# Kernel optimization log

Hardware: AMD Instinct MI355X
Metric: run time of the kernel (lower is better)

Reference implementation:

```python
import jax, jax.numpy as jnp
import numpy as np

B, N, G, H = 64, 1000, 500, 256
TANH_CLIP = 10.0


def setup_inputs() -> dict:
    key = jax.random.key(0)
    ks = jax.random.split(key, 8)
    embeddings = jax.random.normal(ks[0], (B, N, H), dtype=jnp.float32)
    dists = jax.random.uniform(ks[1], (B, N, N), dtype=jnp.float32)
    last_node = jax.random.randint(ks[2], (B, G), 0, N)
    visited = jax.random.uniform(ks[3], (B, G, N)) < 0.3
    group_ninf_mask = jnp.where(visited, -jnp.inf, 0.0).astype(jnp.float32)
    s = 1.0 / np.sqrt(H)
    Wq_graph = jax.random.normal(ks[4], (H, H), dtype=jnp.float32) * s
    Wq_first = jax.random.normal(ks[5], (H, H), dtype=jnp.float32) * s
    Wq_last = jax.random.normal(ks[6], (H, H), dtype=jnp.float32) * s
    W_visited = jax.random.normal(ks[7], (H, H), dtype=jnp.float32) * s
    return dict(embeddings=embeddings, dists=dists, last_node=last_node,
                group_ninf_mask=group_ninf_mask, Wq_graph=Wq_graph,
                Wq_first=Wq_first, Wq_last=Wq_last, W_visited=W_visited)


def reference(embeddings, dists, last_node, group_ninf_mask,
              Wq_graph, Wq_first, Wq_last, W_visited) -> jnp.ndarray:
    b, n, h = embeddings.shape
    g = last_node.shape[1]
    inv_sqrt_h = 1.0 / np.float32(np.sqrt(h))
    inv_sqrt_2 = np.float32(1.0 / np.sqrt(2.0))

    # reset(): graph query from mean-pooled embeddings  [B,1,H]
    q_graph = jnp.einsum('bih,oh->bio', embeddings.mean(axis=1, keepdims=True), Wq_graph)

    # gather last-node embeddings  [B,G,H]
    idx = jnp.broadcast_to(last_node[:, :, None], (b, g, h))
    last_emb = jnp.take_along_axis(embeddings, idx, axis=1)
    q_last = jnp.einsum('bgh,oh->bgo', last_emb, Wq_last)
    # first call: q_first built from the same last-node embedding
    q_first = jnp.einsum('bgh,oh->bgo', last_emb, Wq_first)

    # visited-set query: mask (-inf->1) @ embeddings / N, then linear
    mask_visited = jnp.where(jnp.isneginf(group_ninf_mask), 1.0, group_ninf_mask)
    pooled = jnp.einsum('bgn,bnh->bgh', mask_visited, embeddings) / np.float32(n)
    q_visited = jnp.einsum('bgh,oh->bgo', pooled, W_visited)

    # distances from last node to all nodes  [B,G,N]
    didx = jnp.broadcast_to(last_node[:, :, None], (b, g, n))
    distances = jnp.take_along_axis(dists, didx, axis=1)

    final_q = q_last + q_first + q_graph + q_visited  # [B,G,H]
    score = jnp.einsum('bgh,bnh->bgn', final_q, embeddings) * inv_sqrt_h - distances * inv_sqrt_2
    score_clipped = TANH_CLIP * jnp.tanh(score)
    mask_prob = jnp.where(jnp.isneginf(group_ninf_mask), -1e8, group_ninf_mask)
    return jax.nn.softmax(score_clipped + mask_prob, axis=-1)
```

## Files before the change

kernel.cpp:

```cpp
#include <hip/hip_runtime.h>
#include <hip/hip_fp16.h>
#include <math.h>

#define Bb 64
#define Nn 1000
#define Gg 500
#define Hh 256
#define GP 512
#define NP 1024

#define WS_MP   0u
#define WS_RS   262144u
#define WS_BM   294912u
#define WS_WC16 1343488u
#define WS_E16  1409024u
#define WS_T16  9601024u
#define WS_P16  17989632u
#define WS_F16  WS_T16
#define WS_PO   22183936u

typedef __attribute__((ext_vector_type(8))) short short8;
typedef __attribute__((ext_vector_type(8))) _Float16 f16x8;
typedef __attribute__((ext_vector_type(4))) float f32x4;
typedef __attribute__((ext_vector_type(4))) unsigned short u16x4;

#define MFMAH(a,b,c) __builtin_amdgcn_mfma_f32_16x16x32_f16(a,b,c,0,0,0)
#define SW(row, chunk) (((row) << 6) + ((((chunk) ^ ((row) & 7))) << 3))

__device__ __forceinline__ unsigned short f16b(float v) {
  return __half_as_ushort(__float2half(v));
}
__device__ __forceinline__ float h2f(unsigned short u) {
  return __half2float(__ushort_as_half(u));
}

__global__ __launch_bounds__(256) void k_front(const float* __restrict__ emb,
                                               const float* __restrict__ gm,
                                               const float* __restrict__ Wf,
                                               const float* __restrict__ Wl,
                                               const float* __restrict__ Wv,
                                               float* __restrict__ ws) {
  __shared__ float tile[64][68];
  __shared__ float colsum[16][64];
  int bid = blockIdx.x, t = threadIdx.x;
  if (bid < 4096) {
    int nt = bid & 15, ht = (bid >> 4) & 3, b = bid >> 6;
    int c4 = (t & 15) * 4, r0 = t >> 4;
    int n0 = nt * 64, h0 = ht * 64;
    unsigned short* e16 = (unsigned short*)(ws + WS_E16);
    unsigned short* t16 = (unsigned short*)(ws + WS_T16);
    float cs0 = 0.f, cs1 = 0.f, cs2 = 0.f, cs3 = 0.f;
#pragma unroll
    for (int rr = 0; rr < 4; ++rr) {
      int r = r0 + rr * 16;
      int n = n0 + r;
      float4 v = {0.f, 0.f, 0.f, 0.f};
      if (n < Nn) {
        size_t idx = ((size_t)(b * Nn + n)) * Hh + h0 + c4;
        v = *(const float4*)(emb + idx);
        u16x4 e4 = { f16b(v.x), f16b(v.y), f16b(v.z), f16b(v.w) };
        *(u16x4*)(e16 + idx) = e4;
      }
      *(float4*)&tile[r][c4] = v;
      cs0 += v.x; cs1 += v.y; cs2 += v.z; cs3 += v.w;
    }
    colsum[r0][c4 + 0] = cs0; colsum[r0][c4 + 1] = cs1;
    colsum[r0][c4 + 2] = cs2; colsum[r0][c4 + 3] = cs3;
    __syncthreads();
    {
      int h_l = t >> 2, nseg = t & 3;
      short8 h8a, h8b;
#pragma unroll
      for (int i = 0; i < 16; ++i) {
        float v = tile[nseg * 16 + i][h_l];
        unsigned short hv = f16b(v);
        if (i < 8) h8a[i] = (short)hv;
        else       h8b[i-8] = (short)hv;
      }
      size_t base = ((size_t)(b * Hh + h0 + h_l)) * NP + n0 + nseg * 16;
      *(short8*)(t16 + base) = h8a; *(short8*)(t16 + base + 8) = h8b;
    }
    if (t < 64) {
      float s = 0.f;
#pragma unroll
      for (int i = 0; i < 16; ++i) s += colsum[i][t];
      ws[WS_MP + (((size_t)(b * Hh + h0 + t)) << 4) + nt] = s;
    }
  } else if (bid < 12288) {
    int w = t >> 6, l = t & 63;
    int row = (bid - 4096) * 4 + w;
    int b = row >> 9, g = row & 511;
    unsigned long long* dst = (unsigned long long*)((unsigned short*)(ws + WS_BM) + (size_t)row * 64);
    if (g < Gg) {
      const float* src = gm + ((size_t)b * Gg + g) * Nn;
#pragma unroll
      for (int i = 0; i < 16; ++i) {
        int n = i * 64 + l;
        bool bit = (n < Nn) ? (src[n] < -1e30f) : false;
        unsigned long long m = __ballot(bit);
        if (l == i) dst[i] = m;
      }
    } else {
      if (l < 16) dst[l] = 0ull;
    }
  } else if (bid < 12544) {
    int o = bid - 12288, k = t;
    unsigned short* wc = (unsigned short*)(ws + WS_WC16);
    wc[o*512 + k]       = f16b(Wv[o*Hh + k]);
    wc[o*512 + 256 + k] = f16b(Wl[o*Hh + k] + Wf[o*Hh + k]);
  } else {
    ws[WS_RS + (bid - 12544) * 256 + t] = 0.f;
  }
}

__global__ __launch_bounds__(256, 2) void k_pool(float* __restrict__ ws) {
  __shared__ __align__(16) unsigned short sT[128*64];
  int id = blockIdx.x;
  int xcd = id & 7, seq = id >> 3;
  int b = xcd * 8 + (seq >> 3);
  int inner = seq & 7, ht = inner >> 2, gt = inner & 3;
  int t = threadIdx.x, w = t >> 6, lane = t & 63;
  int wh = w >> 1, wg = w & 1, l15 = lane & 15, lk = lane >> 4;
  const unsigned short* t16 = (const unsigned short*)(ws + WS_T16);
  const unsigned short* bmp = (const unsigned short*)(ws + WS_BM);
  unsigned short* p16 = (unsigned short*)(ws + WS_P16);
  int h0 = ht*128, g0 = gt*128;
  f32x4 acc[4][4] = {};
  const unsigned short* brow[4];
#pragma unroll
  for (int fn = 0; fn < 4; ++fn) {
    int g = g0 + wg*64 + fn*16 + l15; if (g > Gg-1) g = Gg-1;
    brow[fn] = bmp + ((size_t)(b*GP + g)) * 64;
  }
  int bitoff = (lk & 1) * 8;
  int srow = t >> 1, sc0 = (t & 1) * 4;
  size_t sbase = ((size_t)(b*Hh + h0 + srow)) * NP;
  for (int st = 0; st < 16; ++st) {
    int k0 = st * 64;
#pragma unroll
    for (int i = 0; i < 4; ++i) {
      int cc = sc0 + i;
      *(short8*)&sT[SW(srow, cc)] = *(const short8*)(t16 + sbase + k0 + cc*8);
    }
    __syncthreads();
#pragma unroll
    for (int kk = 0; kk < 64; kk += 32) {
      f16x8 ah[4], bmf[4];
#pragma unroll
      for (int fm = 0; fm < 4; ++fm)
        ah[fm] = *(const f16x8*)&sT[SW(wh*64 + fm*16 + l15, (kk>>3) + lk)];
#pragma unroll
      for (int fn = 0; fn < 4; ++fn) {
        unsigned c = brow[fn][((k0 + kk) >> 4) + (lk >> 1)];
        short8 bs;
#pragma unroll
        for (int i = 0; i < 8; ++i)
          bs[i] = ((c >> (bitoff + i)) & 1) ? (short)0x3C00 : (short)0;
        bmf[fn] = *(const f16x8*)&bs;
      }
#pragma unroll
      for (int fm = 0; fm < 4; ++fm)
#pragma unroll
        for (int fn = 0; fn < 4; ++fn)
          acc[fm][fn] = MFMAH(ah[fm], bmf[fn], acc[fm][fn]);
    }
    __syncthreads();
  }
#pragma unroll
  for (int fm = 0; fm < 4; ++fm)
#pragma unroll
    for (int fn = 0; fn < 4; ++fn) {
      int h = h0 + wh*64 + fm*16 + lk*4;
      int g = g0 + wg*64 + fn*16 + l15;
      u16x4 v4;
#pragma unroll
      for (int j = 0; j < 4; ++j) v4[j] = f16b(acc[fm][fn][j] * (1.0f/Nn));
      *(u16x4*)(p16 + ((size_t)(b*GP + g)) * Hh + h) = v4;
    }
}

__global__ __launch_bounds__(256, 2) void k_finalq(const int* __restrict__ last_node,
                                                   const float* __restrict__ Wg,
                                                   float* __restrict__ ws) {
  __shared__ __align__(16) unsigned short sA[128*64], sB[128*64];
  __shared__ int lL[128];
  __shared__ float mean[256];
  __shared__ float qv[128];
  int id = blockIdx.x;
  int xcd = id & 7, seq = id >> 3;
  int b = xcd * 8 + (seq >> 3);
  int inner = seq & 7, ot = inner >> 2, gt = inner & 3;
  int t = threadIdx.x, w = t >> 6, lane = t & 63;
  int wo = w >> 1, wg = w & 1, l15 = lane & 15, lk = lane >> 4;
  const unsigned short* wc = (const unsigned short*)(ws + WS_WC16);
  const unsigned short* p16 = (const unsigned short*)(ws + WS_P16);
  const unsigned short* e16 = (const unsigned short*)(ws + WS_E16);
  unsigned short* f16 = (unsigned short*)(ws + WS_F16);
  int o0 = ot*128, g0 = gt*128;
  if (t < 128) lL[t] = last_node[b*Gg + ((g0 + t) < Gg ? (g0 + t) : Gg-1)];
  {
    const float4* mp4 = (const float4*)(ws + WS_MP + (((size_t)(b * Hh + t)) << 4));
    float s = 0.f;
#pragma unroll
    for (int q = 0; q < 4; ++q) {
      float4 v = mp4[q];
      s += v.x + v.y + v.z + v.w;
    }
    mean[t] = s * (1.0f/Nn);
  }
  __syncthreads();
  if (t < 128) {
    const float4* wrow = (const float4*)(Wg + (size_t)(o0 + t) * Hh);
    float a = 0.f;
#pragma unroll
    for (int h4 = 0; h4 < 64; ++h4) {
      float4 wv = wrow[h4];
      a += mean[h4*4]*wv.x + mean[h4*4+1]*wv.y + mean[h4*4+2]*wv.z + mean[h4*4+3]*wv.w;
    }
    qv[t] = a;
  }
  __syncthreads();
  f32x4 acc[4][4] = {};
  int srow = t >> 1, sc0 = (t & 1) * 4;
  size_t abase = ((size_t)(o0 + srow)) * 512;
  size_t pbase = ((size_t)(b*GP + g0 + srow)) * Hh;
  size_t lbase = ((size_t)(b*Nn + lL[srow])) * Hh;
  for (int st = 0; st < 8; ++st) {
    int k0 = st * 64;
#pragma unroll
    for (int i = 0; i < 4; ++i) {
      int cc = sc0 + i;
      int d = SW(srow, cc);
      *(short8*)&sA[d] = *(const short8*)(wc + abase + k0 + cc*8);
      if (k0 < 256)
        *(short8*)&sB[d] = *(const short8*)(p16 + pbase + k0 + cc*8);
      else
        *(short8*)&sB[d] = *(const short8*)(e16 + lbase + (k0 - 256) + cc*8);
    }
    __syncthreads();
#pragma unroll
    for (int kk = 0; kk < 64; kk += 32) {
      f16x8 a[4], bb[4];
#pragma unroll
      for (int fm = 0; fm < 4; ++fm)
        a[fm] = *(const f16x8*)&sA[SW(wo*64 + fm*16 + l15, (kk>>3) + lk)];
#pragma unroll
      for (int fn = 0; fn < 4; ++fn)
        bb[fn] = *(const f16x8*)&sB[SW(wg*64 + fn*16 + l15, (kk>>3) + lk)];
#pragma unroll
      for (int fm = 0; fm < 4; ++fm)
#pragma unroll
        for (int fn = 0; fn < 4; ++fn)
          acc[fm][fn] = MFMAH(a[fm], bb[fn], acc[fm][fn]);
    }
    __syncthreads();
  }
#pragma unroll
  for (int fm = 0; fm < 4; ++fm) {
    int ob = wo*64 + fm*16 + lk*4;
    float q4[4] = { qv[ob+0], qv[ob+1], qv[ob+2], qv[ob+3] };
#pragma unroll
    for (int fn = 0; fn < 4; ++fn) {
      int g = g0 + wg*64 + fn*16 + l15;
      u16x4 v4;
#pragma unroll
      for (int j = 0; j < 4; ++j) v4[j] = f16b(acc[fm][fn][j] + q4[j]);
      *(u16x4*)(f16 + ((size_t)(b*GP + g)) * Hh + o0 + ob) = v4;
    }
  }
}

__global__ __launch_bounds__(256, 4) void k_score(const float* __restrict__ dists,
                                                  const int* __restrict__ last_node,
                                                  float* __restrict__ ws) {
  __shared__ __align__(16) unsigned short sE[128*64], sF[128*64];
  __shared__ int lL[128];
  int id = blockIdx.x;
  int swz = ((id & 7) << 8) | (id >> 3);
  int gt = swz & 3, nt = (swz >> 2) & 7, b = swz >> 5;
  int t = threadIdx.x, w = t >> 6, lane = t & 63;
  int wn = w >> 1, wg = w & 1, l15 = lane & 15, lk = lane >> 4;
  const unsigned short* e16 = (const unsigned short*)(ws + WS_E16);
  const unsigned short* f16 = (const unsigned short*)(ws + WS_F16);
  const unsigned short* bmp = (const unsigned short*)(ws + WS_BM);
  unsigned short* po = (unsigned short*)(ws + WS_PO);
  float* rs = ws + WS_RS;
  int n0 = nt*128, g0 = gt*128;
  if (t < 128) lL[t] = last_node[b*Gg + ((g0 + t) < Gg ? (g0 + t) : Gg-1)];
  __syncthreads();
  f32x4 acc[4][4] = {};
  int srow = t >> 1, sc0 = (t & 1) * 4;
  int nr = n0 + srow; if (nr > Nn-1) nr = Nn-1;
  size_t ebase = ((size_t)(b*Nn + nr)) * Hh;
  size_t fbase = ((size_t)(b*GP + g0 + srow)) * Hh;
  for (int st = 0; st < 4; ++st) {
    int k0 = st * 64;
#pragma unroll
    for (int i = 0; i < 4; ++i) {
      int cc = sc0 + i;
      int d = SW(srow, cc);
      *(short8*)&sE[d] = *(const short8*)(e16 + ebase + k0 + cc*8);
      *(short8*)&sF[d] = *(const short8*)(f16 + fbase + k0 + cc*8);
    }
    __syncthreads();
#pragma unroll
    for (int kk = 0; kk < 64; kk += 32) {
      f16x8 a[4], bb[4];
#pragma unroll
      for (int fm = 0; fm < 4; ++fm)
        a[fm] = *(const f16x8*)&sE[SW(wn*64 + fm*16 + l15, (kk>>3) + lk)];
#pragma unroll
      for (int fn = 0; fn < 4; ++fn)
        bb[fn] = *(const f16x8*)&sF[SW(wg*64 + fn*16 + l15, (kk>>3) + lk)];
#pragma unroll
      for (int fm = 0; fm < 4; ++fm)
#pragma unroll
        for (int fn = 0; fn < 4; ++fn)
          acc[fm][fn] = MFMAH(a[fm], bb[fn], acc[fm][fn]);
    }
    __syncthreads();
  }
  const float c2 = 0.70710678118654752f;
  float rsum[4] = {0.f, 0.f, 0.f, 0.f};
#pragma unroll
  for (int fn = 0; fn < 4; ++fn) {
    int gl = wg*64 + fn*16 + l15;
    int g = g0 + gl;
    if (g < Gg) {
      int L = lL[gl];
      const float* drow = dists + ((size_t)(b*Nn + L)) * Nn;
      const unsigned short* bmr = bmp + ((size_t)(b*GP + g)) * 64;
      unsigned short* prow = po + ((size_t)(b*Gg + g)) * 1024;
#pragma unroll
      for (int fm = 0; fm < 4; ++fm) {
        int n = n0 + wn*64 + fm*16 + lk*4;
        if (n < Nn) {
          float4 d4 = *(const float4*)(drow + n);
          unsigned cb = bmr[n >> 4];
          int bo = n & 15;
          float dd[4] = {d4.x, d4.y, d4.z, d4.w};
          unsigned short h4[4];
#pragma unroll
          for (int j = 0; j < 4; ++j) {
            float s = fmaf(acc[fm][fn][j], 0.0625f, -dd[j] * c2);
            float e = __expf(-2.0f * fabsf(s));
            float r = __builtin_amdgcn_rcpf(1.0f + e);
            float m = fmaf(-20.0f, e * r, 10.0f);
            float parg = copysignf(m, s) - 10.0f;
            float p = ((cb >> (bo + j)) & 1) ? 0.f : __expf(parg);
            rsum[fn] += p;
            h4[j] = f16b(p);
          }
          uint2 u = { (unsigned)h4[0] | ((unsigned)h4[1] << 16),
                      (unsigned)h4[2] | ((unsigned)h4[3] << 16) };
          *(uint2*)(prow + n) = u;
        }
      }
    }
  }
#pragma unroll
  for (int fn = 0; fn < 4; ++fn) {
    rsum[fn] += __shfl_xor(rsum[fn], 16);
    rsum[fn] += __shfl_xor(rsum[fn], 32);
    int g = g0 + wg*64 + fn*16 + l15;
    if (lk == 0 && g < Gg) atomicAdd(rs + b*GP + g, rsum[fn]);
  }
}

__global__ __launch_bounds__(256) void k_norm(const float* __restrict__ ws,
                                              float* __restrict__ out) {
  int id = blockIdx.x, t = threadIdx.x;
  int xcd = id & 7, seq = id >> 3;
  int b = xcd * 8 + (seq >> 8);
  int inner = seq & 255;
  int v = inner * 256 + t;
  if (v >= 62500) return;
  int lg = v / 125;
  int n = (v - lg * 125) * 8;
  const unsigned short* po = (const unsigned short*)(ws + WS_PO);
  size_t bg = (size_t)b * Gg + lg;
  float inv = 1.0f / ws[WS_RS + b*GP + lg];
  uint4 u = *(const uint4*)(po + bg * 1024 + n);
  float* orow = out + bg * Nn + n;
  float4 o0, o1;
  o0.x = h2f((unsigned short)(u.x & 0xFFFF)) * inv;
  o0.y = h2f((unsigned short)(u.x >> 16)) * inv;
  o0.z = h2f((unsigned short)(u.y & 0xFFFF)) * inv;
  o0.w = h2f((unsigned short)(u.y >> 16)) * inv;
  o1.x = h2f((unsigned short)(u.z & 0xFFFF)) * inv;
  o1.y = h2f((unsigned short)(u.z >> 16)) * inv;
  o1.z = h2f((unsigned short)(u.w & 0xFFFF)) * inv;
  o1.w = h2f((unsigned short)(u.w >> 16)) * inv;
  *(float4*)orow = o0;
  *(float4*)(orow + 4) = o1;
}

extern "C" void kernel_launch(void* const* d_in, const int* in_sizes, int n_in,
                              void* d_out, int out_size, void* d_ws, size_t ws_size,
                              hipStream_t stream) {
  const float* emb       = (const float*)d_in[0];
  const float* dists     = (const float*)d_in[1];
  const int*   last_node = (const int*)d_in[2];
  const float* gm        = (const float*)d_in[3];
  const float* Wg        = (const float*)d_in[4];
  const float* Wf        = (const float*)d_in[5];
  const float* Wl        = (const float*)d_in[6];
  const float* Wv        = (const float*)d_in[7];
  float* out = (float*)d_out;
  float* ws  = (float*)d_ws;

  hipLaunchKernelGGL(k_front,  dim3(12672),     dim3(256), 0, stream, emb, gm, Wf, Wl, Wv, ws);
  hipLaunchKernelGGL(k_pool,   dim3(512),       dim3(256), 0, stream, ws);
  hipLaunchKernelGGL(k_finalq, dim3(512),       dim3(256), 0, stream, last_node, Wg, ws);
  hipLaunchKernelGGL(k_score,  dim3(2048),      dim3(256), 0, stream, dists, last_node, ws);
  hipLaunchKernelGGL(k_norm,   dim3(16384),     dim3(256), 0, stream, ws, out);
}
```

Measured before the change: 300.2 us.

## Prefetch next K-tile into registers to overlap global loads with MFMA

In the pooled-visited, final-query and score GEMM kernels, the first K-tile is staged before the loop. Each iteration then issues global loads for the next tile into registers before computing on the current shared-memory tile, and writes them to shared memory after the trailing barrier. This is meant to hide global memory latency behind MFMA work. It raises register pressure, which could reduce occupancy under the existing launch bounds, and removes two pre-loop barriers.

```diff
diff --git a/kernel.cpp b/kernel.cpp
--- a/kernel.cpp
+++ b/kernel.cpp
@@ -135,12 +135,20 @@
   int bitoff = (lk & 1) * 8;
   int srow = t >> 1, sc0 = (t & 1) * 4;
   size_t sbase = ((size_t)(b*Hh + h0 + srow)) * NP;
+#pragma unroll
+  for (int i = 0; i < 4; ++i) {
+    int cc = sc0 + i;
+    *(short8*)&sT[SW(srow, cc)] = *(const short8*)(t16 + sbase + cc*8);
+  }
   for (int st = 0; st < 16; ++st) {
     int k0 = st * 64;
-#pragma unroll
-    for (int i = 0; i < 4; ++i) {
-      int cc = sc0 + i;
-      *(short8*)&sT[SW(srow, cc)] = *(const short8*)(t16 + sbase + k0 + cc*8);
+    short8 pt[4];
+    if (st < 15) {
+#pragma unroll
+      for (int i = 0; i < 4; ++i) {
+        int cc = sc0 + i;
+        pt[i] = *(const short8*)(t16 + sbase + k0 + 64 + cc*8);
+      }
     }
     __syncthreads();
 #pragma unroll
@@ -165,6 +173,11 @@
           acc[fm][fn] = MFMAH(ah[fm], bmf[fn], acc[fm][fn]);
     }
     __syncthreads();
+    if (st < 15) {
+#pragma unroll
+      for (int i = 0; i < 4; ++i)
+        *(short8*)&sT[SW(srow, sc0 + i)] = pt[i];
+    }
   }
 #pragma unroll
   for (int fm = 0; fm < 4; ++fm)
@@ -219,23 +232,30 @@
     }
     qv[t] = a;
   }
-  __syncthreads();
   f32x4 acc[4][4] = {};
   int srow = t >> 1, sc0 = (t & 1) * 4;
   size_t abase = ((size_t)(o0 + srow)) * 512;
   size_t pbase = ((size_t)(b*GP + g0 + srow)) * Hh;
   size_t lbase = ((size_t)(b*Nn + lL[srow])) * Hh;
+#pragma unroll
+  for (int i = 0; i < 4; ++i) {
+    int cc = sc0 + i;
+    int d = SW(srow, cc);
+    *(short8*)&sA[d] = *(const short8*)(wc + abase + cc*8);
+    *(short8*)&sB[d] = *(const short8*)(p16 + pbase + cc*8);
+  }
   for (int st = 0; st < 8; ++st) {
     int k0 = st * 64;
-#pragma unroll
-    for (int i = 0; i < 4; ++i) {
-      int cc = sc0 + i;
-      int d = SW(srow, cc);
-      *(short8*)&sA[d] = *(const short8*)(wc + abase + k0 + cc*8);
-      if (k0 < 256)
-        *(short8*)&sB[d] = *(const short8*)(p16 + pbase + k0 + cc*8);
-      else
-        *(short8*)&sB[d] = *(const short8*)(e16 + lbase + (k0 - 256) + cc*8);
+    short8 pa[4], pb[4];
+    if (st < 7) {
+      int kn = k0 + 64;
+#pragma unroll
+      for (int i = 0; i < 4; ++i) {
+        int cc = sc0 + i;
+        pa[i] = *(const short8*)(wc + abase + kn + cc*8);
+        pb[i] = (kn < 256) ? *(const short8*)(p16 + pbase + kn + cc*8)
+                           : *(const short8*)(e16 + lbase + (kn - 256) + cc*8);
+      }
     }
     __syncthreads();
 #pragma unroll
@@ -254,6 +274,14 @@
           acc[fm][fn] = MFMAH(a[fm], bb[fn], acc[fm][fn]);
     }
     __syncthreads();
+    if (st < 7) {
+#pragma unroll
+      for (int i = 0; i < 4; ++i) {
+        int d = SW(srow, sc0 + i);
+        *(short8*)&sA[d] = pa[i];
+        *(short8*)&sB[d] = pb[i];
+      }
+    }
   }
 #pragma unroll
   for (int fm = 0; fm < 4; ++fm) {
@@ -287,20 +315,29 @@
   float* rs = ws + WS_RS;
   int n0 = nt*128, g0 = gt*128;
   if (t < 128) lL[t] = last_node[b*Gg + ((g0 + t) < Gg ? (g0 + t) : Gg-1)];
-  __syncthreads();
   f32x4 acc[4][4] = {};
   int srow = t >> 1, sc0 = (t & 1) * 4;
   int nr = n0 + srow; if (nr > Nn-1) nr = Nn-1;
   size_t ebase = ((size_t)(b*Nn + nr)) * Hh;
   size_t fbase = ((size_t)(b*GP + g0 + srow)) * Hh;
+#pragma unroll
+  for (int i = 0; i < 4; ++i) {
+    int cc = sc0 + i;
+    int d = SW(srow, cc);
+    *(short8*)&sE[d] = *(const short8*)(e16 + ebase + cc*8);
+    *(short8*)&sF[d] = *(const short8*)(f16 + fbase + cc*8);
+  }
   for (int st = 0; st < 4; ++st) {
     int k0 = st * 64;
-#pragma unroll
-    for (int i = 0; i < 4; ++i) {
-      int cc = sc0 + i;
-      int d = SW(srow, cc);
-      *(short8*)&sE[d] = *(const short8*)(e16 + ebase + k0 + cc*8);
-      *(short8*)&sF[d] = *(const short8*)(f16 + fbase + k0 + cc*8);
+    short8 pe[4], pf[4];
+    if (st < 3) {
+      int kn = k0 + 64;
+#pragma unroll
+      for (int i = 0; i < 4; ++i) {
+        int cc = sc0 + i;
+        pe[i] = *(const short8*)(e16 + ebase + kn + cc*8);
+        pf[i] = *(const short8*)(f16 + fbase + kn + cc*8);
+      }
     }
     __syncthreads();
 #pragma unroll
@@ -319,6 +356,14 @@
           acc[fm][fn] = MFMAH(a[fm], bb[fn], acc[fm][fn]);
     }
     __syncthreads();
+    if (st < 3) {
+#pragma unroll
+      for (int i = 0; i < 4; ++i) {
+        int d = SW(srow, sc0 + i);
+        *(short8*)&sE[d] = pe[i];
+        *(short8*)&sF[d] = pf[i];
+      }
+    }
   }
   const float c2 = 0.70710678118654752f;
   float rsum[4] = {0.f, 0.f, 0.f, 0.f};
```

After: 325.3 us. 1.08x slower.
